# Kernel tuning notes

Hardware: AMD Instinct MI355X
Metric: run time of the kernel (lower is better)

Reference implementation:

```python
import jax, jax.numpy as jnp
import numpy as np

N_GRAPHS = 128  # number of graphs in the batch (max value of `batch`)
NEG_SLOPE = 0.2  # PyG GATConv default LeakyReLU slope


def gat_conv(x, src, dst, W, att_src, att_dst, bias, concat):
    """PyG-style GATConv (eval mode). x: [N, F_in]; src/dst: [E] (self-loops included)."""
    N = x.shape[0]
    H, C = att_src.shape
    xh = (x @ W).reshape(N, H, C)                      # [N, H, C]
    a_src = jnp.sum(xh * att_src, axis=-1)             # [N, H]
    a_dst = jnp.sum(xh * att_dst, axis=-1)             # [N, H]
    alpha = a_src[src] + a_dst[dst]                    # [E, H] edge scores
    alpha = jax.nn.leaky_relu(alpha, NEG_SLOPE)
    # segment softmax over incoming edges of each dst node
    amax = jax.ops.segment_max(alpha, dst, num_segments=N)   # [N, H]
    e = jnp.exp(alpha - amax[dst])                            # [E, H]
    denom = jax.ops.segment_sum(e, dst, num_segments=N)      # [N, H]
    attn = e / denom[dst]                                     # [E, H]
    msg = xh[src] * attn[:, :, None]                          # [E, H, C]
    out = jax.ops.segment_sum(msg, dst, num_segments=N)      # [N, H, C]
    out = out.reshape(N, H * C) if concat else out.mean(axis=1)
    return out + bias


def setup_inputs():
    key = jax.random.key(0)
    ks = jax.random.split(key, 12)
    N, E, F_in, H, C_hid, C_out = 50000, 800000, 128, 8, 32, 10
    x = jax.random.normal(ks[0], (N, F_in), dtype=jnp.float32)
    edge_index = jax.random.randint(ks[1], (2, E), 0, N, dtype=jnp.int32)
    batch = jnp.sort(jax.random.randint(ks[2], (N,), 0, N_GRAPHS, dtype=jnp.int32))
    s_in = 1.0 / np.sqrt(F_in)
    s_h = 1.0 / np.sqrt(H * C_hid)
    W1 = jax.random.normal(ks[3], (F_in, H * C_hid), dtype=jnp.float32) * s_in
    att_src1 = jax.random.normal(ks[4], (H, C_hid), dtype=jnp.float32) * 0.1
    att_dst1 = jax.random.normal(ks[5], (H, C_hid), dtype=jnp.float32) * 0.1
    b1 = jnp.zeros((H * C_hid,), dtype=jnp.float32)
    W2 = jax.random.normal(ks[6], (H * C_hid, C_out), dtype=jnp.float32) * s_h
    att_src2 = jax.random.normal(ks[7], (1, C_out), dtype=jnp.float32) * 0.1
    att_dst2 = jax.random.normal(ks[8], (1, C_out), dtype=jnp.float32) * 0.1
    b2 = jnp.zeros((C_out,), dtype=jnp.float32)
    return {"x": x, "edge_index": edge_index, "batch": batch,
            "W1": W1, "att_src1": att_src1, "att_dst1": att_dst1, "b1": b1,
            "W2": W2, "att_src2": att_src2, "att_dst2": att_dst2, "b2": b2}


def reference(x, edge_index, batch, W1, att_src1, att_dst1, b1, W2, att_src2, att_dst2, b2):
    N = x.shape[0]
    # PyG GATConv default: add self-loops
    loops = jnp.arange(N, dtype=edge_index.dtype)
    src = jnp.concatenate([edge_index[0], loops])
    dst = jnp.concatenate([edge_index[1], loops])
    # eval mode: dropout(p=0.6) is identity
    h = gat_conv(x, src, dst, W1, att_src1, att_dst1, b1, concat=True)   # [N, H*C_hid]
    h = jax.nn.elu(h)
    h = gat_conv(h, src, dst, W2, att_src2, att_dst2, b2, concat=False)  # [N, C_out]
    h = jax.nn.elu(h)
    # global mean pool over graphs
    sums = jax.ops.segment_sum(h, batch, num_segments=N_GRAPHS)          # [G, C_out]
    counts = jax.ops.segment_sum(jnp.ones((N,), h.dtype), batch, num_segments=N_GRAPHS)
    pooled = sums / jnp.maximum(counts, 1.0)[:, None]
    return jax.nn.log_softmax(pooled, axis=1)
```

## Files before the change

### kernel.cpp

```cpp
#include <hip/hip_runtime.h>

#define N_NODES 50000
#define N_EDGES 800000
#define E_TOT   850000
#define F_IN    128
#define HC      256
#define NH      8
#define C_OUT   10
#define N_GRAPH 128
#define NBLK    49
#define XSTRIDE 16
#define NB_DEG  3322

typedef __attribute__((ext_vector_type(8))) short bf16x8;
typedef __attribute__((ext_vector_type(4))) float f32x4;
typedef __attribute__((ext_vector_type(2))) float f32x2;

__device__ __forceinline__ float lrelu(float x){ return x > 0.f ? x : 0.2f * x; }
__device__ __forceinline__ float elu1(float x){ return x > 0.f ? x : (__expf(x) - 1.f); }

__device__ __forceinline__ unsigned short f2bf(float f){
    unsigned int u = __float_as_uint(f);
    return (unsigned short)((u + 0x7fffu + ((u >> 16) & 1u)) >> 16);
}
__device__ __forceinline__ float bf2f(unsigned short h){
    return __uint_as_float((unsigned int)h << 16);
}
__device__ __forceinline__ unsigned char f2fp8(float v){
    unsigned int t = __builtin_amdgcn_cvt_pk_fp8_f32(v, 0.f, 0, false);
    return (unsigned char)(t & 0xffu);
}

__global__ void k_setup(const int* __restrict__ ei, int* __restrict__ deg,
                        const float* __restrict__ W1, unsigned short* __restrict__ bt,
                        const float* __restrict__ W2, float* __restrict__ W2t){
    int b = blockIdx.x;
    if (b < NB_DEG){
        int e = b * 256 + threadIdx.x;
        if (e < E_TOT){
            int dst = (e < N_EDGES) ? ei[N_EDGES + e] : (e - N_EDGES);
            atomicAdd(deg + dst, 1);
        }
    } else if (b < NB_DEG + 128){
        int k = b - NB_DEG;
        int c = threadIdx.x;
        float v = W1[k * HC + c];
        unsigned short hi = f2bf(v);
        unsigned short lo = f2bf(v - bf2f(hi));
        bt[(size_t)c * 256 + k]       = hi;
        bt[(size_t)c * 256 + 128 + k] = lo;
    } else {
        for (int j = threadIdx.x; j < HC * C_OUT; j += 256){
            int k = j / C_OUT, c = j % C_OUT;
            W2t[c * HC + k] = W2[j];
        }
    }
}

__global__ __launch_bounds__(256) void k_gemm1m(const float* __restrict__ x,
                                                const unsigned short* __restrict__ bt,
                                                const float* __restrict__ atts,
                                                const float* __restrict__ attd,
                                                unsigned int* __restrict__ xhb,
                                                float* __restrict__ a_s,
                                                float* __restrict__ a_d){
    __shared__ unsigned char tile[4][32][264];
    __shared__ float sc[4][32][8], dc[4][32][8];
    const int wave = threadIdx.x >> 6, lane = threadIdx.x & 63;
    const int quad = lane >> 4, lidx = lane & 15;
    const int m0 = blockIdx.x * 128 + wave * 32;
    int ar0 = m0 + lidx;      if (ar0 >= N_NODES) ar0 = N_NODES - 1;
    int ar1 = m0 + 16 + lidx; if (ar1 >= N_NODES) ar1 = N_NODES - 1;

    bf16x8 ah0[4], al0[4], ah1[4], al1[4];
    #pragma unroll
    for (int ks = 0; ks < 4; ks++){
        const float* p0 = x + (size_t)ar0 * F_IN + ks * 32 + quad * 8;
        const float* p1 = x + (size_t)ar1 * F_IN + ks * 32 + quad * 8;
        float4 u0 = *(const float4*)p0, u1 = *(const float4*)(p0 + 4);
        float4 w0 = *(const float4*)p1, w1 = *(const float4*)(p1 + 4);
        float v0[8] = {u0.x,u0.y,u0.z,u0.w,u1.x,u1.y,u1.z,u1.w};
        float v1[8] = {w0.x,w0.y,w0.z,w0.w,w1.x,w1.y,w1.z,w1.w};
        bf16x8 h0v, l0v, h1v, l1v;
        #pragma unroll
        for (int j = 0; j < 8; j++){
            unsigned short hh = f2bf(v0[j]);
            h0v[j] = (short)hh;
            l0v[j] = (short)f2bf(v0[j] - bf2f(hh));
            unsigned short hg = f2bf(v1[j]);
            h1v[j] = (short)hg;
            l1v[j] = (short)f2bf(v1[j] - bf2f(hg));
        }
        ah0[ks] = h0v; al0[ks] = l0v; ah1[ks] = h1v; al1[ks] = l1v;
    }

    const uint4* bbase = (const uint4*)bt;
    bf16x8 bh[4], bl[4];
    {
        const uint4* bcol = bbase + (size_t)lidx * 32 + quad;
        #pragma unroll
        for (int ks = 0; ks < 4; ks++){
            bh[ks] = __builtin_bit_cast(bf16x8, bcol[ks * 4]);
            bl[ks] = __builtin_bit_cast(bf16x8, bcol[16 + ks * 4]);
        }
    }
    for (int h = 0; h < NH; h++){
        float ss0[4] = {0,0,0,0}, ss1[4] = {0,0,0,0};
        float dd0[4] = {0,0,0,0}, dd1[4] = {0,0,0,0};
        #pragma unroll
        for (int sub = 0; sub < 2; sub++){
            int col = h * 32 + sub * 16 + lidx;
            bf16x8 nh[4], nl[4];
            int tn = h * 2 + sub + 1;
            if (tn < 16){
                int ncol = (tn >> 1) * 32 + (tn & 1) * 16 + lidx;
                const uint4* nb = bbase + (size_t)ncol * 32 + quad;
                #pragma unroll
                for (int ks = 0; ks < 4; ks++){
                    nh[ks] = __builtin_bit_cast(bf16x8, nb[ks * 4]);
                    nl[ks] = __builtin_bit_cast(bf16x8, nb[16 + ks * 4]);
                }
            }
            f32x4 a0A = {0.f,0.f,0.f,0.f}, a0B = {0.f,0.f,0.f,0.f}, a0C = {0.f,0.f,0.f,0.f};
            f32x4 a1A = {0.f,0.f,0.f,0.f}, a1B = {0.f,0.f,0.f,0.f}, a1C = {0.f,0.f,0.f,0.f};
            #pragma unroll
            for (int ks = 0; ks < 4; ks++){
                a0A = __builtin_amdgcn_mfma_f32_16x16x32_bf16(ah0[ks], bh[ks], a0A, 0, 0, 0);
                a1A = __builtin_amdgcn_mfma_f32_16x16x32_bf16(ah1[ks], bh[ks], a1A, 0, 0, 0);
                a0B = __builtin_amdgcn_mfma_f32_16x16x32_bf16(ah0[ks], bl[ks], a0B, 0, 0, 0);
                a1B = __builtin_amdgcn_mfma_f32_16x16x32_bf16(ah1[ks], bl[ks], a1B, 0, 0, 0);
                a0C = __builtin_amdgcn_mfma_f32_16x16x32_bf16(al0[ks], bh[ks], a0C, 0, 0, 0);
                a1C = __builtin_amdgcn_mfma_f32_16x16x32_bf16(al1[ks], bh[ks], a1C, 0, 0, 0);
            }
            f32x4 acc0, acc1;
            #pragma unroll
            for (int reg = 0; reg < 4; reg++){
                acc0[reg] = (a0A[reg] + a0B[reg]) + a0C[reg];
                acc1[reg] = (a1A[reg] + a1B[reg]) + a1C[reg];
            }
            float sv = atts[col], dv = attd[col];
            #pragma unroll
            for (int reg = 0; reg < 4; reg++){
                tile[wave][quad*4+reg][col]    = f2fp8(acc0[reg]);
                tile[wave][16+quad*4+reg][col] = f2fp8(acc1[reg]);
                ss0[reg] += acc0[reg] * sv;  dd0[reg] += acc0[reg] * dv;
                ss1[reg] += acc1[reg] * sv;  dd1[reg] += acc1[reg] * dv;
            }
            #pragma unroll
            for (int ks = 0; ks < 4; ks++){ bh[ks] = nh[ks]; bl[ks] = nl[ks]; }
        }
        #pragma unroll
        for (int reg = 0; reg < 4; reg++){
            float a = ss0[reg], b = dd0[reg], c = ss1[reg], d = dd1[reg];
            a += __shfl_xor(a,1,64); a += __shfl_xor(a,2,64); a += __shfl_xor(a,4,64); a += __shfl_xor(a,8,64);
            b += __shfl_xor(b,1,64); b += __shfl_xor(b,2,64); b += __shfl_xor(b,4,64); b += __shfl_xor(b,8,64);
            c += __shfl_xor(c,1,64); c += __shfl_xor(c,2,64); c += __shfl_xor(c,4,64); c += __shfl_xor(c,8,64);
            d += __shfl_xor(d,1,64); d += __shfl_xor(d,2,64); d += __shfl_xor(d,4,64); d += __shfl_xor(d,8,64);
            if (lidx == 0){
                sc[wave][quad*4+reg][h]    = a;  dc[wave][quad*4+reg][h]    = b;
                sc[wave][16+quad*4+reg][h] = c;  dc[wave][16+quad*4+reg][h] = d;
            }
        }
    }
    __syncthreads();
    for (int r = 0; r < 32; r++){
        int row = m0 + r;
        if (row < N_NODES){
            unsigned int p = *(const unsigned int*)&tile[wave][r][lane * 4];
            xhb[(size_t)row * 64 + lane] = p;
        }
    }
    {
        int linear = lane * 4;
        int row = m0 + (linear >> 3);
        if (row < N_NODES){
            const float* sb = &sc[wave][0][0];
            const float* db = &dc[wave][0][0];
            float4 s4 = *(const float4*)(sb + linear);
            float4 d4 = *(const float4*)(db + linear);
            *(float4*)(a_s + (size_t)m0 * NH + linear) = s4;
            *(float4*)(a_d + (size_t)m0 * NH + linear) = d4;
        }
    }
}

__global__ void k_bsum(const int* __restrict__ deg, int* __restrict__ bsum, int* __restrict__ rowp){
    int b = blockIdx.x;
    int v = 0;
    for (int i = threadIdx.x; i < 1024; i += 256){
        int idx = b * 1024 + i;
        if (idx < N_NODES) v += deg[idx];
    }
    #pragma unroll
    for (int off = 1; off < 64; off <<= 1) v += __shfl_xor(v, off, 64);
    __shared__ int sd[4];
    if ((threadIdx.x & 63) == 0) sd[threadIdx.x >> 6] = v;
    __syncthreads();
    if (threadIdx.x == 0){
        bsum[b] = sd[0] + sd[1] + sd[2] + sd[3];
        if (b == 0) rowp[N_NODES] = E_TOT;
    }
}

__global__ __launch_bounds__(1024) void k_scan(const int* __restrict__ deg, const int* __restrict__ bsum,
                                               int* __restrict__ rowp, int* __restrict__ cur){
    __shared__ int sd[1024];
    int b = blockIdx.x;
    int bex = 0;
    for (int j = 0; j < b; j++) bex += bsum[j];
    int i = b * 1024 + threadIdx.x;
    int v = (i < N_NODES) ? deg[i] : 0;
    sd[threadIdx.x] = v;
    __syncthreads();
    for (int off = 1; off < 1024; off <<= 1){
        int t = (threadIdx.x >= off) ? sd[threadIdx.x - off] : 0;
        __syncthreads();
        sd[threadIdx.x] += t;
        __syncthreads();
    }
    if (i < N_NODES){
        int excl = sd[threadIdx.x] - v + bex;
        rowp[i] = excl;
        cur[i]  = excl;
    }
}

__global__ void k_scatter(const int* __restrict__ ei, int* __restrict__ cur, int* __restrict__ col){
    int e = blockIdx.x * 256 + threadIdx.x;
    if (e >= E_TOT) return;
    int s, d;
    if (e < N_EDGES){ s = ei[e]; d = ei[N_EDGES + e]; }
    else { s = e - N_EDGES; d = s; }
    int slot = atomicAdd(cur + d, 1);
    col[slot] = s;
}

__global__ __launch_bounds__(256) void k_agg1f(const unsigned int* __restrict__ xhb,
                                               const float* __restrict__ a_s, const float* __restrict__ a_d,
                                               const int* __restrict__ rowp, const int* __restrict__ colb,
                                               const float* __restrict__ b1, const float* __restrict__ W2t,
                                               const float* __restrict__ as2, const float* __restrict__ ad2,
                                               float* __restrict__ xh2){
    int wave = threadIdx.x >> 6, lane = threadIdx.x & 63;
    int half = lane >> 5, l32 = lane & 31;
    int n = blockIdx.x * 8 + wave * 2 + half;
    int h = l32 >> 2;
    float adh = a_d[(unsigned)(n * NH + h)];
    int s0 = rowp[n], s1 = rowp[n + 1];
    const uint2* xv = (const uint2*)xhb;
    float a0=0.f,a1=0.f,a2=0.f,a3=0.f,a4=0.f,a5=0.f,a6=0.f,a7=0.f;
    float den = 0.f;
    int idx = s0;
    for (; idx + 3 < s1; idx += 4){
        int sA = colb[idx], sB = colb[idx+1], sC = colb[idx+2], sD = colb[idx+3];
        float eA = a_s[(unsigned)(sA * NH + h)];
        float eB = a_s[(unsigned)(sB * NH + h)];
        float eC = a_s[(unsigned)(sC * NH + h)];
        float eD = a_s[(unsigned)(sD * NH + h)];
        uint2 pA = xv[(unsigned)(sA * 32 + l32)];
        uint2 pB = xv[(unsigned)(sB * 32 + l32)];
        uint2 pC = xv[(unsigned)(sC * 32 + l32)];
        uint2 pD = xv[(unsigned)(sD * 32 + l32)];
        float wA = __expf(lrelu(eA + adh));
        float wB = __expf(lrelu(eB + adh));
        float wC = __expf(lrelu(eC + adh));
        float wD = __expf(lrelu(eD + adh));
        den += (wA + wB) + (wC + wD);
        f32x2 q0, q1, q2, q3;
        q0 = __builtin_amdgcn_cvt_pk_f32_fp8(pA.x, false); q1 = __builtin_amdgcn_cvt_pk_f32_fp8(pA.x, true);
        q2 = __builtin_amdgcn_cvt_pk_f32_fp8(pA.y, false); q3 = __builtin_amdgcn_cvt_pk_f32_fp8(pA.y, true);
        a0 += wA*q0[0]; a1 += wA*q0[1]; a2 += wA*q1[0]; a3 += wA*q1[1];
        a4 += wA*q2[0]; a5 += wA*q2[1]; a6 += wA*q3[0]; a7 += wA*q3[1];
        q0 = __builtin_amdgcn_cvt_pk_f32_fp8(pB.x, false); q1 = __builtin_amdgcn_cvt_pk_f32_fp8(pB.x, true);
        q2 = __builtin_amdgcn_cvt_pk_f32_fp8(pB.y, false); q3 = __builtin_amdgcn_cvt_pk_f32_fp8(pB.y, true);
        a0 += wB*q0[0]; a1 += wB*q0[1]; a2 += wB*q1[0]; a3 += wB*q1[1];
        a4 += wB*q2[0]; a5 += wB*q2[1]; a6 += wB*q3[0]; a7 += wB*q3[1];
        q0 = __builtin_amdgcn_cvt_pk_f32_fp8(pC.x, false); q1 = __builtin_amdgcn_cvt_pk_f32_fp8(pC.x, true);
        q2 = __builtin_amdgcn_cvt_pk_f32_fp8(pC.y, false); q3 = __builtin_amdgcn_cvt_pk_f32_fp8(pC.y, true);
        a0 += wC*q0[0]; a1 += wC*q0[1]; a2 += wC*q1[0]; a3 += wC*q1[1];
        a4 += wC*q2[0]; a5 += wC*q2[1]; a6 += wC*q3[0]; a7 += wC*q3[1];
        q0 = __builtin_amdgcn_cvt_pk_f32_fp8(pD.x, false); q1 = __builtin_amdgcn_cvt_pk_f32_fp8(pD.x, true);
        q2 = __builtin_amdgcn_cvt_pk_f32_fp8(pD.y, false); q3 = __builtin_amdgcn_cvt_pk_f32_fp8(pD.y, true);
        a0 += wD*q0[0]; a1 += wD*q0[1]; a2 += wD*q1[0]; a3 += wD*q1[1];
        a4 += wD*q2[0]; a5 += wD*q2[1]; a6 += wD*q3[0]; a7 += wD*q3[1];
    }
    for (; idx < s1; idx++){
        int sA = colb[idx];
        float wA = __expf(lrelu(a_s[(unsigned)(sA * NH + h)] + adh));
        den += wA;
        uint2 pA = xv[(unsigned)(sA * 32 + l32)];
        f32x2 q0 = __builtin_amdgcn_cvt_pk_f32_fp8(pA.x, false);
        f32x2 q1 = __builtin_amdgcn_cvt_pk_f32_fp8(pA.x, true);
        f32x2 q2 = __builtin_amdgcn_cvt_pk_f32_fp8(pA.y, false);
        f32x2 q3 = __builtin_amdgcn_cvt_pk_f32_fp8(pA.y, true);
        a0 += wA*q0[0]; a1 += wA*q0[1]; a2 += wA*q1[0]; a3 += wA*q1[1];
        a4 += wA*q2[0]; a5 += wA*q2[1]; a6 += wA*q3[0]; a7 += wA*q3[1];
    }
    float rden = 1.f / den;
    const float4* b4 = (const float4*)b1;
    float4 bb0 = b4[l32 * 2], bb1 = b4[l32 * 2 + 1];
    float r0 = elu1(a0 * rden + bb0.x);
    float r1 = elu1(a1 * rden + bb0.y);
    float r2 = elu1(a2 * rden + bb0.z);
    float r3 = elu1(a3 * rden + bb0.w);
    float r4 = elu1(a4 * rden + bb1.x);
    float r5 = elu1(a5 * rden + bb1.y);
    float r6 = elu1(a6 * rden + bb1.z);
    float r7 = elu1(a7 * rden + bb1.w);
    float o[C_OUT];
    #pragma unroll
    for (int c = 0; c < C_OUT; c++){
        const float4* w4 = (const float4*)(W2t + c * HC);
        float4 w0 = w4[l32 * 2], w1 = w4[l32 * 2 + 1];
        float v = r0*w0.x + r1*w0.y + r2*w0.z + r3*w0.w
                + r4*w1.x + r5*w1.y + r6*w1.z + r7*w1.w;
        v += __shfl_xor(v, 1, 64); v += __shfl_xor(v, 2, 64); v += __shfl_xor(v, 4, 64);
        v += __shfl_xor(v, 8, 64); v += __shfl_xor(v, 16, 64);
        o[c] = v;
    }
    if (l32 == 0){
        float s2 = 0.f, d2 = 0.f;
        #pragma unroll
        for (int c = 0; c < C_OUT; c++){ s2 += o[c] * as2[c]; d2 += o[c] * ad2[c]; }
        float* xr = xh2 + (unsigned)(n * XSTRIDE);
        *(float4*)(xr)     = make_float4(o[0], o[1], o[2], o[3]);
        *(float4*)(xr + 4) = make_float4(o[4], o[5], o[6], o[7]);
        *(float4*)(xr + 8) = make_float4(o[8], o[9], s2, d2);
    }
}

__global__ __launch_bounds__(256) void k_agg2(const float* __restrict__ xh2,
                                              const int* __restrict__ rowp, const int* __restrict__ colb,
                                              const float* __restrict__ b2,
                                              float* __restrict__ h2){
    int grp = threadIdx.x >> 4, l16 = threadIdx.x & 15;
    int n = blockIdx.x * 16 + grp;
    if (n >= N_NODES) return;
    float adn = xh2[(unsigned)(n * XSTRIDE + 11)];
    int s0 = rowp[n], s1 = rowp[n + 1];
    float acc[C_OUT] = {};
    float den = 0.f;
    for (int idx = s0 + l16; idx < s1; idx += 16){
        int s = colb[idx];
        const float* xr = xh2 + (unsigned)(s * XSTRIDE);
        float4 q0 = *(const float4*)(xr);
        float4 q1 = *(const float4*)(xr + 4);
        float4 q2 = *(const float4*)(xr + 8);
        float w = __expf(lrelu(q2.z + adn));
        den += w;
        acc[0] += w*q0.x; acc[1] += w*q0.y; acc[2] += w*q0.z; acc[3] += w*q0.w;
        acc[4] += w*q1.x; acc[5] += w*q1.y; acc[6] += w*q1.z; acc[7] += w*q1.w;
        acc[8] += w*q2.x; acc[9] += w*q2.y;
    }
    #pragma unroll
    for (int off = 1; off < 16; off <<= 1){
        den += __shfl_xor(den, off, 64);
        #pragma unroll
        for (int c = 0; c < C_OUT; c++) acc[c] += __shfl_xor(acc[c], off, 64);
    }
    if (l16 == 0){
        float rden = 1.f / den;
        #pragma unroll
        for (int c = 0; c < C_OUT; c++)
            h2[(unsigned)(n * C_OUT + c)] = elu1(acc[c] * rden + b2[c]);
    }
}

__global__ __launch_bounds__(256) void k_pool(const float* __restrict__ h2, const int* __restrict__ batch,
                                              float* __restrict__ out){
    int g = blockIdx.x;
    int l = 0, r = N_NODES;
    while (l < r){ int m = (l + r) >> 1; if (batch[m] < g) l = m + 1; else r = m; }
    int lo = l;
    l = 0; r = N_NODES;
    while (l < r){ int m = (l + r) >> 1; if (batch[m] < g + 1) l = m + 1; else r = m; }
    int hi = l;
    float acc[C_OUT] = {};
    for (int i = lo + (int)threadIdx.x; i < hi; i += 256){
        const float* row = h2 + (size_t)i * C_OUT;
        #pragma unroll
        for (int c = 0; c < C_OUT; c++) acc[c] += row[c];
    }
    #pragma unroll
    for (int c = 0; c < C_OUT; c++){
        #pragma unroll
        for (int off = 32; off > 0; off >>= 1) acc[c] += __shfl_xor(acc[c], off, 64);
    }
    __shared__ float sd[4][C_OUT];
    int wave = threadIdx.x >> 6, lane = threadIdx.x & 63;
    if (lane == 0){
        #pragma unroll
        for (int c = 0; c < C_OUT; c++) sd[wave][c] = acc[c];
    }
    __syncthreads();
    if (threadIdx.x == 0){
        float cnt = (float)(hi - lo);
        if (cnt < 1.f) cnt = 1.f;
        float v[C_OUT];
        float m = -1e30f;
        #pragma unroll
        for (int c = 0; c < C_OUT; c++){
            v[c] = (sd[0][c] + sd[1][c] + sd[2][c] + sd[3][c]) / cnt;
            m = fmaxf(m, v[c]);
        }
        float sum = 0.f;
        #pragma unroll
        for (int c = 0; c < C_OUT; c++) sum += __expf(v[c] - m);
        float lse = m + __logf(sum);
        #pragma unroll
        for (int c = 0; c < C_OUT; c++) out[g * C_OUT + c] = v[c] - lse;
    }
}

extern "C" void kernel_launch(void* const* d_in, const int* in_sizes, int n_in,
                              void* d_out, int out_size, void* d_ws, size_t ws_size,
                              hipStream_t stream){
    const float* x    = (const float*)d_in[0];
    const int*   ei   = (const int*)d_in[1];
    const int*   batch= (const int*)d_in[2];
    const float* W1   = (const float*)d_in[3];
    const float* as1  = (const float*)d_in[4];
    const float* ad1  = (const float*)d_in[5];
    const float* b1   = (const float*)d_in[6];
    const float* W2   = (const float*)d_in[7];
    const float* as2v = (const float*)d_in[8];
    const float* ad2v = (const float*)d_in[9];
    const float* b2   = (const float*)d_in[10];
    float* out = (float*)d_out;

    char* ws = (char*)d_ws;
    size_t off = 0;
    auto alloc = [&](size_t bytes)->char*{
        char* p = ws + off;
        off = (off + bytes + 255) & ~(size_t)255;
        return p;
    };
    unsigned int* xhb  = (unsigned int*)alloc((size_t)N_NODES * HC);
    unsigned short* bt = (unsigned short*)alloc((size_t)HC * 256 * 2);
    float* asc1 = (float*)alloc((size_t)N_NODES * NH * 4);
    float* adc1 = (float*)alloc((size_t)N_NODES * NH * 4);
    int*   deg  = (int*)alloc((size_t)N_NODES * 4);
    int*   rowp = (int*)alloc((size_t)(N_NODES + 1) * 4);
    int*   cur  = (int*)alloc((size_t)N_NODES * 4);
    int*   colb = (int*)alloc((size_t)E_TOT * 4);
    int*   bsum = (int*)alloc(64 * 4);
    float* xh2  = (float*)alloc((size_t)N_NODES * XSTRIDE * 4);
    float* W2t  = (float*)alloc((size_t)HC * C_OUT * 4);
    float* h2   = (float*)alloc((size_t)N_NODES * C_OUT * 4);
    (void)ws_size; (void)in_sizes; (void)n_in; (void)out_size;

    hipMemsetAsync(deg, 0, (size_t)N_NODES * 4, stream);
    hipLaunchKernelGGL(k_setup,   dim3(NB_DEG + 129), dim3(256), 0, stream, ei, deg, W1, bt, W2, W2t);
    hipLaunchKernelGGL(k_gemm1m,  dim3(391),   dim3(256), 0, stream, x, bt, as1, ad1, xhb, asc1, adc1);
    hipLaunchKernelGGL(k_bsum,    dim3(NBLK),  dim3(256), 0, stream, deg, bsum, rowp);
    hipLaunchKernelGGL(k_scan,    dim3(NBLK),  dim3(1024),0, stream, deg, bsum, rowp, cur);
    hipLaunchKernelGGL(k_scatter, dim3((E_TOT + 255)/256), dim3(256), 0, stream, ei, cur, colb);
    hipLaunchKernelGGL(k_agg1f,   dim3(N_NODES / 8), dim3(256), 0, stream, xhb, asc1, adc1, rowp, colb, b1, W2t, as2v, ad2v, xh2);
    hipLaunchKernelGGL(k_agg2,    dim3((N_NODES + 15)/16), dim3(256), 0, stream, xh2, rowp, colb, b2, h2);
    hipLaunchKernelGGL(k_pool,    dim3(N_GRAPH), dim3(256), 0, stream, h2, batch, out);
}
```

Baseline: 295.1 us.

## Split GEMM heads across wave pairs and pack agg1 accumulation into f32x2

```diff
diff --git a/kernel.cpp b/kernel.cpp
--- a/kernel.cpp
+++ b/kernel.cpp
@@ -64,11 +64,13 @@
                                                 unsigned int* __restrict__ xhb,
                                                 float* __restrict__ a_s,
                                                 float* __restrict__ a_d){
-    __shared__ unsigned char tile[4][32][264];
-    __shared__ float sc[4][32][8], dc[4][32][8];
+    __shared__ unsigned char tile[2][32][264];
+    __shared__ float sc[2][32][8], dc[2][32][8];
     const int wave = threadIdx.x >> 6, lane = threadIdx.x & 63;
+    const int pair = wave >> 1;
+    const int h0 = (wave & 1) * 4;
     const int quad = lane >> 4, lidx = lane & 15;
-    const int m0 = blockIdx.x * 128 + wave * 32;
+    const int m0 = blockIdx.x * 64 + pair * 32;
     int ar0 = m0 + lidx;      if (ar0 >= N_NODES) ar0 = N_NODES - 1;
     int ar1 = m0 + 16 + lidx; if (ar1 >= N_NODES) ar1 = N_NODES - 1;
 
@@ -95,31 +97,19 @@
     }
 
     const uint4* bbase = (const uint4*)bt;
-    bf16x8 bh[4], bl[4];
-    {
-        const uint4* bcol = bbase + (size_t)lidx * 32 + quad;
-        #pragma unroll
-        for (int ks = 0; ks < 4; ks++){
-            bh[ks] = __builtin_bit_cast(bf16x8, bcol[ks * 4]);
-            bl[ks] = __builtin_bit_cast(bf16x8, bcol[16 + ks * 4]);
-        }
-    }
-    for (int h = 0; h < NH; h++){
+    for (int hh = 0; hh < 4; hh++){
+        const int h = h0 + hh;
         float ss0[4] = {0,0,0,0}, ss1[4] = {0,0,0,0};
         float dd0[4] = {0,0,0,0}, dd1[4] = {0,0,0,0};
         #pragma unroll
         for (int sub = 0; sub < 2; sub++){
             int col = h * 32 + sub * 16 + lidx;
-            bf16x8 nh[4], nl[4];
-            int tn = h * 2 + sub + 1;
-            if (tn < 16){
-                int ncol = (tn >> 1) * 32 + (tn & 1) * 16 + lidx;
-                const uint4* nb = bbase + (size_t)ncol * 32 + quad;
-                #pragma unroll
-                for (int ks = 0; ks < 4; ks++){
-                    nh[ks] = __builtin_bit_cast(bf16x8, nb[ks * 4]);
-                    nl[ks] = __builtin_bit_cast(bf16x8, nb[16 + ks * 4]);
-                }
+            const uint4* bcol = bbase + (size_t)col * 32 + quad;
+            bf16x8 bh[4], bl[4];
+            #pragma unroll
+            for (int ks = 0; ks < 4; ks++){
+                bh[ks] = __builtin_bit_cast(bf16x8, bcol[ks * 4]);
+                bl[ks] = __builtin_bit_cast(bf16x8, bcol[16 + ks * 4]);
             }
             f32x4 a0A = {0.f,0.f,0.f,0.f}, a0B = {0.f,0.f,0.f,0.f}, a0C = {0.f,0.f,0.f,0.f};
             f32x4 a1A = {0.f,0.f,0.f,0.f}, a1B = {0.f,0.f,0.f,0.f}, a1C = {0.f,0.f,0.f,0.f};
@@ -141,13 +131,11 @@
             float sv = atts[col], dv = attd[col];
             #pragma unroll
             for (int reg = 0; reg < 4; reg++){
-                tile[wave][quad*4+reg][col]    = f2fp8(acc0[reg]);
-                tile[wave][16+quad*4+reg][col] = f2fp8(acc1[reg]);
+                tile[pair][quad*4+reg][col]    = f2fp8(acc0[reg]);
+                tile[pair][16+quad*4+reg][col] = f2fp8(acc1[reg]);
                 ss0[reg] += acc0[reg] * sv;  dd0[reg] += acc0[reg] * dv;
                 ss1[reg] += acc1[reg] * sv;  dd1[reg] += acc1[reg] * dv;
             }
-            #pragma unroll
-            for (int ks = 0; ks < 4; ks++){ bh[ks] = nh[ks]; bl[ks] = nl[ks]; }
         }
         #pragma unroll
         for (int reg = 0; reg < 4; reg++){
@@ -157,29 +145,30 @@
             c += __shfl_xor(c,1,64); c += __shfl_xor(c,2,64); c += __shfl_xor(c,4,64); c += __shfl_xor(c,8,64);
             d += __shfl_xor(d,1,64); d += __shfl_xor(d,2,64); d += __shfl_xor(d,4,64); d += __shfl_xor(d,8,64);
             if (lidx == 0){
-                sc[wave][quad*4+reg][h]    = a;  dc[wave][quad*4+reg][h]    = b;
-                sc[wave][16+quad*4+reg][h] = c;  dc[wave][16+quad*4+reg][h] = d;
+                sc[pair][quad*4+reg][h]    = a;  dc[pair][quad*4+reg][h]    = b;
+                sc[pair][16+quad*4+reg][h] = c;  dc[pair][16+quad*4+reg][h] = d;
             }
         }
     }
     __syncthreads();
-    for (int r = 0; r < 32; r++){
-        int row = m0 + r;
+    const int rbase = (wave & 1) * 16;
+    for (int r = 0; r < 16; r++){
+        int row = m0 + rbase + r;
         if (row < N_NODES){
-            unsigned int p = *(const unsigned int*)&tile[wave][r][lane * 4];
+            unsigned int p = *(const unsigned int*)&tile[pair][rbase + r][lane * 4];
             xhb[(size_t)row * 64 + lane] = p;
         }
     }
     {
-        int linear = lane * 4;
-        int row = m0 + (linear >> 3);
+        int linear = lane * 2;
+        int row = m0 + rbase + (linear >> 3);
         if (row < N_NODES){
-            const float* sb = &sc[wave][0][0];
-            const float* db = &dc[wave][0][0];
-            float4 s4 = *(const float4*)(sb + linear);
-            float4 d4 = *(const float4*)(db + linear);
-            *(float4*)(a_s + (size_t)m0 * NH + linear) = s4;
-            *(float4*)(a_d + (size_t)m0 * NH + linear) = d4;
+            const float* sb = &sc[pair][rbase][0];
+            const float* db = &dc[pair][rbase][0];
+            float2 s2 = *(const float2*)(sb + linear);
+            float2 d2 = *(const float2*)(db + linear);
+            *(float2*)(a_s + (size_t)row * NH + (linear & 7)) = s2;
+            *(float2*)(a_d + (size_t)row * NH + (linear & 7)) = d2;
         }
     }
 }
@@ -248,7 +237,7 @@
     float adh = a_d[(unsigned)(n * NH + h)];
     int s0 = rowp[n], s1 = rowp[n + 1];
     const uint2* xv = (const uint2*)xhb;
-    float a0=0.f,a1=0.f,a2=0.f,a3=0.f,a4=0.f,a5=0.f,a6=0.f,a7=0.f;
+    f32x2 a01 = {0.f,0.f}, a23 = {0.f,0.f}, a45 = {0.f,0.f}, a67 = {0.f,0.f};
     float den = 0.f;
     int idx = s0;
     for (; idx + 3 < s1; idx += 4){
@@ -266,47 +255,50 @@
         float wC = __expf(lrelu(eC + adh));
         float wD = __expf(lrelu(eD + adh));
         den += (wA + wB) + (wC + wD);
-        f32x2 q0, q1, q2, q3;
-        q0 = __builtin_amdgcn_cvt_pk_f32_fp8(pA.x, false); q1 = __builtin_amdgcn_cvt_pk_f32_fp8(pA.x, true);
-        q2 = __builtin_amdgcn_cvt_pk_f32_fp8(pA.y, false); q3 = __builtin_amdgcn_cvt_pk_f32_fp8(pA.y, true);
-        a0 += wA*q0[0]; a1 += wA*q0[1]; a2 += wA*q1[0]; a3 += wA*q1[1];
-        a4 += wA*q2[0]; a5 += wA*q2[1]; a6 += wA*q3[0]; a7 += wA*q3[1];
-        q0 = __builtin_amdgcn_cvt_pk_f32_fp8(pB.x, false); q1 = __builtin_amdgcn_cvt_pk_f32_fp8(pB.x, true);
-        q2 = __builtin_amdgcn_cvt_pk_f32_fp8(pB.y, false); q3 = __builtin_amdgcn_cvt_pk_f32_fp8(pB.y, true);
-        a0 += wB*q0[0]; a1 += wB*q0[1]; a2 += wB*q1[0]; a3 += wB*q1[1];
-        a4 += wB*q2[0]; a5 += wB*q2[1]; a6 += wB*q3[0]; a7 += wB*q3[1];
-        q0 = __builtin_amdgcn_cvt_pk_f32_fp8(pC.x, false); q1 = __builtin_amdgcn_cvt_pk_f32_fp8(pC.x, true);
-        q2 = __builtin_amdgcn_cvt_pk_f32_fp8(pC.y, false); q3 = __builtin_amdgcn_cvt_pk_f32_fp8(pC.y, true);
-        a0 += wC*q0[0]; a1 += wC*q0[1]; a2 += wC*q1[0]; a3 += wC*q1[1];
-        a4 += wC*q2[0]; a5 += wC*q2[1]; a6 += wC*q3[0]; a7 += wC*q3[1];
-        q0 = __builtin_amdgcn_cvt_pk_f32_fp8(pD.x, false); q1 = __builtin_amdgcn_cvt_pk_f32_fp8(pD.x, true);
-        q2 = __builtin_amdgcn_cvt_pk_f32_fp8(pD.y, false); q3 = __builtin_amdgcn_cvt_pk_f32_fp8(pD.y, true);
-        a0 += wD*q0[0]; a1 += wD*q0[1]; a2 += wD*q1[0]; a3 += wD*q1[1];
-        a4 += wD*q2[0]; a5 += wD*q2[1]; a6 += wD*q3[0]; a7 += wD*q3[1];
+        f32x2 w2;
+        w2[0] = wA; w2[1] = wA;
+        a01 += w2 * __builtin_amdgcn_cvt_pk_f32_fp8(pA.x, false);
+        a23 += w2 * __builtin_amdgcn_cvt_pk_f32_fp8(pA.x, true);
+        a45 += w2 * __builtin_amdgcn_cvt_pk_f32_fp8(pA.y, false);
+        a67 += w2 * __builtin_amdgcn_cvt_pk_f32_fp8(pA.y, true);
+        w2[0] = wB; w2[1] = wB;
+        a01 += w2 * __builtin_amdgcn_cvt_pk_f32_fp8(pB.x, false);
+        a23 += w2 * __builtin_amdgcn_cvt_pk_f32_fp8(pB.x, true);
+        a45 += w2 * __builtin_amdgcn_cvt_pk_f32_fp8(pB.y, false);
+        a67 += w2 * __builtin_amdgcn_cvt_pk_f32_fp8(pB.y, true);
+        w2[0] = wC; w2[1] = wC;
+        a01 += w2 * __builtin_amdgcn_cvt_pk_f32_fp8(pC.x, false);
+        a23 += w2 * __builtin_amdgcn_cvt_pk_f32_fp8(pC.x, true);
+        a45 += w2 * __builtin_amdgcn_cvt_pk_f32_fp8(pC.y, false);
+        a67 += w2 * __builtin_amdgcn_cvt_pk_f32_fp8(pC.y, true);
+        w2[0] = wD; w2[1] = wD;
+        a01 += w2 * __builtin_amdgcn_cvt_pk_f32_fp8(pD.x, false);
+        a23 += w2 * __builtin_amdgcn_cvt_pk_f32_fp8(pD.x, true);
+        a45 += w2 * __builtin_amdgcn_cvt_pk_f32_fp8(pD.y, false);
+        a67 += w2 * __builtin_amdgcn_cvt_pk_f32_fp8(pD.y, true);
     }
     for (; idx < s1; idx++){
         int sA = colb[idx];
         float wA = __expf(lrelu(a_s[(unsigned)(sA * NH + h)] + adh));
         den += wA;
         uint2 pA = xv[(unsigned)(sA * 32 + l32)];
-        f32x2 q0 = __builtin_amdgcn_cvt_pk_f32_fp8(pA.x, false);
-        f32x2 q1 = __builtin_amdgcn_cvt_pk_f32_fp8(pA.x, true);
-        f32x2 q2 = __builtin_amdgcn_cvt_pk_f32_fp8(pA.y, false);
-        f32x2 q3 = __builtin_amdgcn_cvt_pk_f32_fp8(pA.y, true);
-        a0 += wA*q0[0]; a1 += wA*q0[1]; a2 += wA*q1[0]; a3 += wA*q1[1];
-        a4 += wA*q2[0]; a5 += wA*q2[1]; a6 += wA*q3[0]; a7 += wA*q3[1];
+        f32x2 w2; w2[0] = wA; w2[1] = wA;
+        a01 += w2 * __builtin_amdgcn_cvt_pk_f32_fp8(pA.x, false);
+        a23 += w2 * __builtin_amdgcn_cvt_pk_f32_fp8(pA.x, true);
+        a45 += w2 * __builtin_amdgcn_cvt_pk_f32_fp8(pA.y, false);
+        a67 += w2 * __builtin_amdgcn_cvt_pk_f32_fp8(pA.y, true);
     }
     float rden = 1.f / den;
     const float4* b4 = (const float4*)b1;
     float4 bb0 = b4[l32 * 2], bb1 = b4[l32 * 2 + 1];
-    float r0 = elu1(a0 * rden + bb0.x);
-    float r1 = elu1(a1 * rden + bb0.y);
-    float r2 = elu1(a2 * rden + bb0.z);
-    float r3 = elu1(a3 * rden + bb0.w);
-    float r4 = elu1(a4 * rden + bb1.x);
-    float r5 = elu1(a5 * rden + bb1.y);
-    float r6 = elu1(a6 * rden + bb1.z);
-    float r7 = elu1(a7 * rden + bb1.w);
+    float r0 = elu1(a01[0] * rden + bb0.x);
+    float r1 = elu1(a01[1] * rden + bb0.y);
+    float r2 = elu1(a23[0] * rden + bb0.z);
+    float r3 = elu1(a23[1] * rden + bb0.w);
+    float r4 = elu1(a45[0] * rden + bb1.x);
+    float r5 = elu1(a45[1] * rden + bb1.y);
+    float r6 = elu1(a67[0] * rden + bb1.z);
+    float r7 = elu1(a67[1] * rden + bb1.w);
     float o[C_OUT];
     #pragma unroll
     for (int c = 0; c < C_OUT; c++){
@@ -451,7 +443,7 @@
 
     hipMemsetAsync(deg, 0, (size_t)N_NODES * 4, stream);
     hipLaunchKernelGGL(k_setup,   dim3(NB_DEG + 129), dim3(256), 0, stream, ei, deg, W1, bt, W2, W2t);
-    hipLaunchKernelGGL(k_gemm1m,  dim3(391),   dim3(256), 0, stream, x, bt, as1, ad1, xhb, asc1, adc1);
+    hipLaunchKernelGGL(k_gemm1m,  dim3(782),   dim3(256), 0, stream, x, bt, as1, ad1, xhb, asc1, adc1);
     hipLaunchKernelGGL(k_bsum,    dim3(NBLK),  dim3(256), 0, stream, deg, bsum, rowp);
     hipLaunchKernelGGL(k_scan,    dim3(NBLK),  dim3(1024),0, stream, deg, bsum, rowp, cur);
     hipLaunchKernelGGL(k_scatter, dim3((E_TOT + 255)/256), dim3(256), 0, stream, ei, cur, colb);
```

New measurement: 300.7 us. Within noise of the previous version (+1.9%).
